# Kernel tuning notes

Measured on AMD Instinct MI355X. Metric: run time of the kernel, lower is better.

## Reference

```python
import jax, jax.numpy as jnp
import numpy as np

HIDDEN = 1024
CUTOFFS = (0, 20000, 60000, 200000)  # 3 clusters
N_CLUSTER = len(CUTOFFS) - 1
EMB_DIMS = (HIDDEN, HIDDEN // 2, HIDDEN // 4)  # div_val=2


def setup_inputs() -> dict:
    key = jax.random.key(0)
    ks = jax.random.split(key, 6)
    s = 0.02  # init scale for weights
    x = jax.random.normal(ks[0], (2, 512, HIDDEN), dtype=jnp.float32)
    # head: Linear(hidden, cutoffs[1] + n_cluster - 1, bias=False) -> weight [out, in]
    W_head = jax.random.normal(ks[1], (CUTOFFS[1] + N_CLUSTER - 1, HIDDEN), dtype=jnp.float32) * s
    # cluster 1: proj hidden->512, tail 512 -> 40000
    W_proj1 = jax.random.normal(ks[2], (EMB_DIMS[1], HIDDEN), dtype=jnp.float32) * s
    W_tail1 = jax.random.normal(ks[3], (CUTOFFS[2] - CUTOFFS[1], EMB_DIMS[1]), dtype=jnp.float32) * s
    # cluster 2: proj hidden->256, tail 256 -> 140000
    W_proj2 = jax.random.normal(ks[4], (EMB_DIMS[2], HIDDEN), dtype=jnp.float32) * s
    W_tail2 = jax.random.normal(ks[5], (CUTOFFS[3] - CUTOFFS[2], EMB_DIMS[2]), dtype=jnp.float32) * s
    return {"x": x, "W_head": W_head, "W_proj1": W_proj1, "W_tail1": W_tail1,
            "W_proj2": W_proj2, "W_tail2": W_tail2}


def reference(x, W_head, W_proj1, W_tail1, W_proj2, W_tail2):
    # head: [b, s, cutoffs[1] + n_cluster - 1]
    head = jnp.einsum('bsh,vh->bsv', x, W_head)
    head_word_logits = head[..., :CUTOFFS[1]]          # [b, s, 20000] raw logits
    cluster_logits = head[..., CUTOFFS[1]:]            # [b, s, 2]

    # tail cluster 1
    proj1 = jnp.einsum('bsh,eh->bse', x, W_proj1)      # [b, s, 512]
    tail1 = jnp.einsum('bse,ve->bsv', proj1, W_tail1)  # [b, s, 40000]
    tail1 = cluster_logits[..., 0:1] + jax.nn.log_softmax(tail1, axis=-1)

    # tail cluster 2
    proj2 = jnp.einsum('bsh,eh->bse', x, W_proj2)      # [b, s, 256]
    tail2 = jnp.einsum('bse,ve->bsv', proj2, W_tail2)  # [b, s, 140000]
    tail2 = cluster_logits[..., 1:2] + jax.nn.log_softmax(tail2, axis=-1)

    return jnp.concatenate([head_word_logits, tail1, tail2], axis=-1)  # [b, s, 200000]
```

## Files before the change

### kernel.cpp

```cpp
#include <hip/hip_runtime.h>
#include <hip/hip_bf16.h>

typedef __attribute__((ext_vector_type(8))) __bf16 bf16x8;
typedef __attribute__((ext_vector_type(4))) float f32x4;

#define OUTC   200000
#define NHEAD  20002
#define NW1    40000
#define NW2    140000
#define MROWS  1024
#define HID    1024

__device__ __forceinline__ unsigned short f2bf(float f) {
  union { float f; unsigned u; } a; a.f = f;
  unsigned u = a.u;
  return (unsigned short)((u + 0x7fffu + ((u >> 16) & 1u)) >> 16);
}

__global__ void cvt_kernel(const float* __restrict__ in, unsigned short* __restrict__ o, int n4) {
  int i = blockIdx.x * blockDim.x + threadIdx.x;
  if (i >= n4) return;
  float4 v = ((const float4*)in)[i];
  ushort4 r;
  r.x = f2bf(v.x); r.y = f2bf(v.y); r.z = f2bf(v.z); r.w = f2bf(v.w);
  ((ushort4*)o)[i] = r;
}

__device__ __forceinline__ void load16(const unsigned short* g, unsigned short* l) {
  __builtin_amdgcn_global_load_lds(
      (const __attribute__((address_space(1))) unsigned int*)g,
      (__attribute__((address_space(3))) unsigned int*)l, 16, 0, 0);
}

template<int EPI>
__launch_bounds__(256)
__global__ void gemm_bt(const unsigned short* __restrict__ A,
                        const unsigned short* __restrict__ B,
                        int N, int K,
                        float* __restrict__ out,
                        unsigned short* __restrict__ bout,
                        float* __restrict__ cluster,
                        float2* __restrict__ stats,
                        int cbase) {
  __shared__ unsigned short As[128 * 64];
  __shared__ unsigned short Bs[128 * 64];
  __shared__ float sred[128 * 4];

  const int tid  = threadIdx.x;
  const int lane = tid & 63;
  const int w    = tid >> 6;
  const int wm   = w >> 1, wn = w & 1;
  const int l15  = lane & 15, quad = lane >> 4;
  const int mtile = blockIdx.y, ntile = blockIdx.x;
  const int row0 = mtile * 128, col0 = ntile * 128;

  const int srow = tid >> 3;
  const int sgrp = tid & 7;

  f32x4 acc[4][4] = {};

  for (int k0 = 0; k0 < K; k0 += 64) {
#pragma unroll
    for (int p = 0; p < 4; ++p) {
      int r = p * 32 + srow;
      int c = ((sgrp ^ (r & 7)) << 3);
      load16(A + (size_t)(row0 + r) * K + k0 + c, As + (size_t)(p * 256 + tid) * 8);
    }
#pragma unroll
    for (int p = 0; p < 4; ++p) {
      int r = p * 32 + srow;
      int gn = col0 + r; if (gn > N - 1) gn = N - 1;
      int c = ((sgrp ^ (r & 7)) << 3);
      load16(B + (size_t)gn * K + k0 + c, Bs + (size_t)(p * 256 + tid) * 8);
    }
    __syncthreads();
#pragma unroll
    for (int ks = 0; ks < 64; ks += 32) {
      bf16x8 af[4], bfr[4];
#pragma unroll
      for (int i = 0; i < 4; ++i) {
        int r = wm * 64 + i * 16 + l15;
        int g = (ks >> 3) + quad;
        af[i] = *(const bf16x8*)(As + r * 64 + ((g ^ (r & 7)) << 3));
      }
#pragma unroll
      for (int j = 0; j < 4; ++j) {
        int n = wn * 64 + j * 16 + l15;
        int g = (ks >> 3) + quad;
        bfr[j] = *(const bf16x8*)(Bs + n * 64 + ((g ^ (n & 7)) << 3));
      }
#pragma unroll
      for (int i = 0; i < 4; ++i)
#pragma unroll
        for (int j = 0; j < 4; ++j)
          acc[i][j] = __builtin_amdgcn_mfma_f32_16x16x32_bf16(af[i], bfr[j], acc[i][j], 0, 0, 0);
    }
    __syncthreads();
  }

  if (EPI == 0) {
#pragma unroll
    for (int i = 0; i < 4; ++i)
#pragma unroll
      for (int comp = 0; comp < 4; ++comp) {
        int r = row0 + wm * 64 + i * 16 + quad * 4 + comp;
#pragma unroll
        for (int j = 0; j < 4; ++j) {
          int c = col0 + wn * 64 + j * 16 + l15;
          float v = acc[i][j][comp];
          if (c < 20000) out[(size_t)r * OUTC + c] = v;
          else if (c < NHEAD) cluster[r * 2 + (c - 20000)] = v;
        }
      }
  } else if (EPI == 1) {
#pragma unroll
    for (int i = 0; i < 4; ++i)
#pragma unroll
      for (int comp = 0; comp < 4; ++comp) {
        int r = row0 + wm * 64 + i * 16 + quad * 4 + comp;
#pragma unroll
        for (int j = 0; j < 4; ++j) {
          int c = col0 + wn * 64 + j * 16 + l15;
          bout[(size_t)r * N + c] = f2bf(acc[i][j][comp]);
        }
      }
  } else {
#pragma unroll
    for (int i = 0; i < 4; ++i)
#pragma unroll
      for (int comp = 0; comp < 4; ++comp) {
        int r = row0 + wm * 64 + i * 16 + quad * 4 + comp;
        float vv[4];
        float m = -INFINITY;
#pragma unroll
        for (int j = 0; j < 4; ++j) {
          int c = col0 + wn * 64 + j * 16 + l15;
          float v = acc[i][j][comp];
          vv[j] = v;
          if (c < N) { out[(size_t)r * OUTC + cbase + c] = v; m = fmaxf(m, v); }
        }
#pragma unroll
        for (int off = 1; off < 16; off <<= 1) m = fmaxf(m, __shfl_xor(m, off, 64));
        float s = 0.f;
#pragma unroll
        for (int j = 0; j < 4; ++j) {
          int c = col0 + wn * 64 + j * 16 + l15;
          if (c < N) s += __expf(vv[j] - m);
        }
#pragma unroll
        for (int off = 1; off < 16; off <<= 1) s += __shfl_xor(s, off, 64);
        if (l15 == 0) {
          int rt = wm * 64 + i * 16 + quad * 4 + comp;
          sred[(rt * 2 + wn) * 2 + 0] = m;
          sred[(rt * 2 + wn) * 2 + 1] = s;
        }
      }
    __syncthreads();
    if (tid < 128) {
      float m0 = sred[(tid * 2 + 0) * 2 + 0], l0 = sred[(tid * 2 + 0) * 2 + 1];
      float m1 = sred[(tid * 2 + 1) * 2 + 0], l1 = sred[(tid * 2 + 1) * 2 + 1];
      float mm = fmaxf(m0, m1);
      float ll = (m0 == -INFINITY ? 0.f : l0 * __expf(m0 - mm)) +
                 (m1 == -INFINITY ? 0.f : l1 * __expf(m1 - mm));
      stats[(size_t)ntile * 1024 + row0 + tid] = make_float2(mm, ll);
    }
  }
}

__global__ void merge_stats(const float2* __restrict__ stats, int T,
                            const float* __restrict__ cluster, int ci,
                            float* __restrict__ scal) {
  int r = blockIdx.x * 4 + (threadIdx.x >> 6);
  int lane = threadIdx.x & 63;
  float m = -INFINITY, l = 0.f;
  for (int t = lane; t < T; t += 64) {
    float2 s = stats[(size_t)t * 1024 + r];
    float mn = fmaxf(m, s.x);
    l = l * __expf(m - mn) + s.y * __expf(s.x - mn);
    m = mn;
  }
  for (int off = 1; off < 64; off <<= 1) {
    float mo = __shfl_xor(m, off, 64);
    float lo = __shfl_xor(l, off, 64);
    float mn = fmaxf(m, mo);
    l = l * __expf(m - mn) + lo * __expf(mo - mn);
    m = mn;
  }
  if (lane == 0) scal[r] = cluster[r * 2 + ci] - m - logf(l);
}

__global__ void fixup(float* __restrict__ out, const float* __restrict__ s1,
                      const float* __restrict__ s2) {
  int r = blockIdx.y;
  int c4 = blockIdx.x * blockDim.x + threadIdx.x;
  if (c4 >= 45000) return;
  float s = (c4 < 10000) ? s1[r] : s2[r];
  float4* p = (float4*)(out + (size_t)r * OUTC + 20000);
  float4 v = p[c4];
  v.x += s; v.y += s; v.z += s; v.w += s;
  p[c4] = v;
}

extern "C" void kernel_launch(void* const* d_in, const int* in_sizes, int n_in,
                              void* d_out, int out_size, void* d_ws, size_t ws_size,
                              hipStream_t stream) {
  const float* x   = (const float*)d_in[0];
  const float* Wh  = (const float*)d_in[1];
  const float* Wp1 = (const float*)d_in[2];
  const float* Wt1 = (const float*)d_in[3];
  const float* Wp2 = (const float*)d_in[4];
  const float* Wt2 = (const float*)d_in[5];
  float* out = (float*)d_out;

  char* ws = (char*)d_ws;
  size_t off = 0;
  auto alloc = [&](size_t bytes) {
    void* p = ws + off;
    off += (bytes + 255) & ~(size_t)255;
    return p;
  };
  unsigned short* xb   = (unsigned short*)alloc((size_t)MROWS * HID * 2);
  unsigned short* whb  = (unsigned short*)alloc((size_t)NHEAD * HID * 2);
  unsigned short* wp1b = (unsigned short*)alloc((size_t)512 * HID * 2);
  unsigned short* wt1b = (unsigned short*)alloc((size_t)NW1 * 512 * 2);
  unsigned short* wp2b = (unsigned short*)alloc((size_t)256 * HID * 2);
  unsigned short* wt2b = (unsigned short*)alloc((size_t)NW2 * 256 * 2);
  unsigned short* p1b  = (unsigned short*)alloc((size_t)MROWS * 512 * 2);
  unsigned short* p2b  = (unsigned short*)alloc((size_t)MROWS * 256 * 2);
  float*  cluster = (float*)alloc((size_t)MROWS * 2 * 4);
  float2* stats1  = (float2*)alloc((size_t)313 * 1024 * 8);
  float2* stats2  = (float2*)alloc((size_t)1094 * 1024 * 8);
  float*  scal1   = (float*)alloc(1024 * 4);
  float*  scal2   = (float*)alloc(1024 * 4);

  auto cvt = [&](const float* src, unsigned short* dst, size_t n) {
    int n4 = (int)(n / 4);
    cvt_kernel<<<(n4 + 255) / 256, 256, 0, stream>>>(src, dst, n4);
  };
  cvt(x,   xb,   (size_t)MROWS * HID);
  cvt(Wh,  whb,  (size_t)NHEAD * HID);
  cvt(Wp1, wp1b, (size_t)512 * HID);
  cvt(Wt1, wt1b, (size_t)NW1 * 512);
  cvt(Wp2, wp2b, (size_t)256 * HID);
  cvt(Wt2, wt2b, (size_t)NW2 * 256);

  gemm_bt<0><<<dim3(157, 8), 256, 0, stream>>>(xb, whb, NHEAD, HID, out, nullptr, cluster, nullptr, 0);
  gemm_bt<1><<<dim3(4, 8), 256, 0, stream>>>(xb, wp1b, 512, HID, nullptr, p1b, nullptr, nullptr, 0);
  gemm_bt<1><<<dim3(2, 8), 256, 0, stream>>>(xb, wp2b, 256, HID, nullptr, p2b, nullptr, nullptr, 0);
  gemm_bt<2><<<dim3(313, 8), 256, 0, stream>>>(p1b, wt1b, NW1, 512, out, nullptr, nullptr, stats1, 20000);
  gemm_bt<2><<<dim3(1094, 8), 256, 0, stream>>>(p2b, wt2b, NW2, 256, out, nullptr, nullptr, stats2, 60000);
  merge_stats<<<256, 256, 0, stream>>>(stats1, 313, cluster, 0, scal1);
  merge_stats<<<256, 256, 0, stream>>>(stats2, 1094, cluster, 1, scal2);
  fixup<<<dim3(176, 1024), 256, 0, stream>>>(out, scal1, scal2);
}
```

Before: 1.702 ms.

## Recompute tail GEMMs to write final log-softmax output in one pass

The first tail GEMM pass now computes only the per-tile softmax statistics and no longer writes logits. A second GEMM pass recomputes the logits and writes them with the per-row offset already added, which replaces the read-modify-write fixup over the 180000-column tail region. The grid is also transposed so that the eight row tiles sharing a weight tile run next to each other, improving reuse of the B tile in cache. The cost is doing the tail GEMMs twice.

```diff
diff --git a/kernel.cpp b/kernel.cpp
--- a/kernel.cpp
+++ b/kernel.cpp
@@ -41,6 +41,7 @@
                         unsigned short* __restrict__ bout,
                         float* __restrict__ cluster,
                         float2* __restrict__ stats,
+                        const float* __restrict__ scal,
                         int cbase) {
   __shared__ unsigned short As[128 * 64];
   __shared__ unsigned short Bs[128 * 64];
@@ -51,7 +52,7 @@
   const int w    = tid >> 6;
   const int wm   = w >> 1, wn = w & 1;
   const int l15  = lane & 15, quad = lane >> 4;
-  const int mtile = blockIdx.y, ntile = blockIdx.x;
+  const int mtile = blockIdx.x, ntile = blockIdx.y;
   const int row0 = mtile * 128, col0 = ntile * 128;
 
   const int srow = tid >> 3;
@@ -124,12 +125,11 @@
           bout[(size_t)r * N + c] = f2bf(acc[i][j][comp]);
         }
       }
-  } else {
-#pragma unroll
-    for (int i = 0; i < 4; ++i)
-#pragma unroll
-      for (int comp = 0; comp < 4; ++comp) {
-        int r = row0 + wm * 64 + i * 16 + quad * 4 + comp;
+  } else if (EPI == 2) {
+#pragma unroll
+    for (int i = 0; i < 4; ++i)
+#pragma unroll
+      for (int comp = 0; comp < 4; ++comp) {
         float vv[4];
         float m = -INFINITY;
 #pragma unroll
@@ -137,7 +137,7 @@
           int c = col0 + wn * 64 + j * 16 + l15;
           float v = acc[i][j][comp];
           vv[j] = v;
-          if (c < N) { out[(size_t)r * OUTC + cbase + c] = v; m = fmaxf(m, v); }
+          if (c < N) m = fmaxf(m, v);
         }
 #pragma unroll
         for (int off = 1; off < 16; off <<= 1) m = fmaxf(m, __shfl_xor(m, off, 64));
@@ -164,6 +164,19 @@
                  (m1 == -INFINITY ? 0.f : l1 * __expf(m1 - mm));
       stats[(size_t)ntile * 1024 + row0 + tid] = make_float2(mm, ll);
     }
+  } else {
+#pragma unroll
+    for (int i = 0; i < 4; ++i)
+#pragma unroll
+      for (int comp = 0; comp < 4; ++comp) {
+        int r = row0 + wm * 64 + i * 16 + quad * 4 + comp;
+        float s = scal[r];
+#pragma unroll
+        for (int j = 0; j < 4; ++j) {
+          int c = col0 + wn * 64 + j * 16 + l15;
+          if (c < N) out[(size_t)r * OUTC + cbase + c] = acc[i][j][comp] + s;
+        }
+      }
   }
 }
 
@@ -187,18 +200,6 @@
     m = mn;
   }
   if (lane == 0) scal[r] = cluster[r * 2 + ci] - m - logf(l);
-}
-
-__global__ void fixup(float* __restrict__ out, const float* __restrict__ s1,
-                      const float* __restrict__ s2) {
-  int r = blockIdx.y;
-  int c4 = blockIdx.x * blockDim.x + threadIdx.x;
-  if (c4 >= 45000) return;
-  float s = (c4 < 10000) ? s1[r] : s2[r];
-  float4* p = (float4*)(out + (size_t)r * OUTC + 20000);
-  float4 v = p[c4];
-  v.x += s; v.y += s; v.z += s; v.w += s;
-  p[c4] = v;
 }
 
 extern "C" void kernel_launch(void* const* d_in, const int* in_sizes, int n_in,
@@ -244,12 +245,13 @@
   cvt(Wp2, wp2b, (size_t)256 * HID);
   cvt(Wt2, wt2b, (size_t)NW2 * 256);
 
-  gemm_bt<0><<<dim3(157, 8), 256, 0, stream>>>(xb, whb, NHEAD, HID, out, nullptr, cluster, nullptr, 0);
-  gemm_bt<1><<<dim3(4, 8), 256, 0, stream>>>(xb, wp1b, 512, HID, nullptr, p1b, nullptr, nullptr, 0);
-  gemm_bt<1><<<dim3(2, 8), 256, 0, stream>>>(xb, wp2b, 256, HID, nullptr, p2b, nullptr, nullptr, 0);
-  gemm_bt<2><<<dim3(313, 8), 256, 0, stream>>>(p1b, wt1b, NW1, 512, out, nullptr, nullptr, stats1, 20000);
-  gemm_bt<2><<<dim3(1094, 8), 256, 0, stream>>>(p2b, wt2b, NW2, 256, out, nullptr, nullptr, stats2, 60000);
+  gemm_bt<0><<<dim3(8, 157), 256, 0, stream>>>(xb, whb, NHEAD, HID, out, nullptr, cluster, nullptr, nullptr, 0);
+  gemm_bt<1><<<dim3(8, 4), 256, 0, stream>>>(xb, wp1b, 512, HID, nullptr, p1b, nullptr, nullptr, nullptr, 0);
+  gemm_bt<1><<<dim3(8, 2), 256, 0, stream>>>(xb, wp2b, 256, HID, nullptr, p2b, nullptr, nullptr, nullptr, 0);
+  gemm_bt<2><<<dim3(8, 313), 256, 0, stream>>>(p1b, wt1b, NW1, 512, nullptr, nullptr, nullptr, stats1, nullptr, 0);
+  gemm_bt<2><<<dim3(8, 1094), 256, 0, stream>>>(p2b, wt2b, NW2, 256, nullptr, nullptr, nullptr, stats2, nullptr, 0);
   merge_stats<<<256, 256, 0, stream>>>(stats1, 313, cluster, 0, scal1);
   merge_stats<<<256, 256, 0, stream>>>(stats2, 1094, cluster, 1, scal2);
-  fixup<<<dim3(176, 1024), 256, 0, stream>>>(out, scal1, scal2);
-}
+  gemm_bt<3><<<dim3(8, 313), 256, 0, stream>>>(p1b, wt1b, NW1, 512, out, nullptr, nullptr, nullptr, scal1, 20000);
+  gemm_bt<3><<<dim3(8, 1094), 256, 0, stream>>>(p2b, wt2b, NW2, 256, out, nullptr, nullptr, nullptr, scal2, 60000);
+}
```

After: 1.617 ms. -5.0%, faster.
